# Optimization experiments

Hardware: AMD Instinct MI355X
Metric: run time of the kernel (lower is better)

## Reference

```python
import jax, jax.numpy as jnp
import numpy as np


def setup_inputs() -> dict:
    key = jax.random.key(0)
    k1, k2 = jax.random.split(key)
    x = jax.random.normal(k1, (32, 64, 32, 32), dtype=jnp.float32)
    codebook = jax.random.normal(k2, (2048, 64), dtype=jnp.float32)
    return {"x": x, "codebook": codebook}


def reference(x, codebook):
    B, C, H, W = x.shape
    # (B, C, H, W) -> (B*H*W, C) channels-last flatten
    xf = jnp.transpose(x, (0, 2, 3, 1)).reshape(-1, C)
    d2 = (jnp.sum(xf * xf, axis=-1, keepdims=True)
          + jnp.sum(codebook * codebook, axis=-1)[None, :]
          - 2.0 * jnp.einsum('nc,kc->nk', xf, codebook))
    idx = jnp.argmin(d2, axis=-1)            # (B*H*W,)
    quant = codebook[idx]                    # (B*H*W, C)
    commitment_loss = jnp.mean((jax.lax.stop_gradient(quant) - xf) ** 2)
    codebook_loss = jnp.mean((quant - jax.lax.stop_gradient(xf)) ** 2)
    # Straight-through estimator
    quant_ste = xf + jax.lax.stop_gradient(quant - xf)
    quant_out = jnp.transpose(quant_ste.reshape(B, H, W, C), (0, 3, 1, 2))
    min_encoding_indices = idx.reshape(B, H, W)
    return quant_out, codebook_loss, commitment_loss, min_encoding_indices
```

## Files before the change

### kernel.cpp

```cpp
#include <hip/hip_runtime.h>

#define NROWS    32768
#define KENT     2048
#define OUT_Q_SZ 2097152
#define N_ELEMS  2097152.0f
#define THR      1e-4f
#define KLO      0.001953125f

typedef _Float16 f16x8 __attribute__((ext_vector_type(8)));
typedef float    f32x4 __attribute__((ext_vector_type(4)));

#define WS_LOSS  0
#define WS_CNT   4
#define WS_EN    1024
#define WS_LIST  16384
#define WS_PM1   262144
#define WS_PIX   1310720
#define WS_PM2   2359296

__global__ void vq_norms_kernel(const float* __restrict__ cb, float* __restrict__ ws) {
    int e = blockIdx.x * 256 + threadIdx.x;
    if (e == 0) { ws[0] = 0.0f; ((unsigned*)ws)[1] = 0u; }
    if (e < KENT) {
        const float4* row = (const float4*)(cb + e * 64);
        float s = 0.0f;
#pragma unroll
        for (int i = 0; i < 16; ++i) {
            float4 v = row[i];
            s += v.x * v.x + v.y * v.y + v.z * v.z + v.w * v.w;
        }
        *((float*)((char*)ws + WS_EN) + e) = s;
    }
}

__global__ __launch_bounds__(256, 2) void vq_main_kernel(
    const float* __restrict__ x, const float* __restrict__ cb,
    float* __restrict__ ws)
{
    __shared__ f16x8 a_hi[16 * 2 * 64];
    __shared__ f16x8 a_lo[16 * 2 * 64];
    __shared__ float en_s[256];

    const float*  en  = (const float*)((char*)ws + WS_EN);
    float*        pm1 = (float*)((char*)ws + WS_PM1);
    int*          pix = (int*)  ((char*)ws + WS_PIX);
    float*        pm2 = (float*)((char*)ws + WS_PM2);

    const int tid = threadIdx.x;
    const int rg  = blockIdx.x >> 3;
    const int oct = blockIdx.x & 7;

#pragma unroll
    for (int u = 0; u < 8; ++u) {
        int unit = u * 256 + tid;
        int tile = unit >> 7, step = (unit >> 6) & 1, ln = unit & 63;
        int e  = oct * 256 + tile * 16 + (ln & 15);
        int k0 = step * 32 + ((ln >> 4) << 3);
        float4 v0 = *(const float4*)(cb + e * 64 + k0);
        float4 v1 = *(const float4*)(cb + e * 64 + k0 + 4);
        float vv[8] = {v0.x, v0.y, v0.z, v0.w, v1.x, v1.y, v1.z, v1.w};
        f16x8 h, l;
#pragma unroll
        for (int j = 0; j < 8; ++j) {
            _Float16 hi = (_Float16)vv[j];
            float lo = (vv[j] - (float)hi) * 1024.0f;
            h[j] = hi; l[j] = (_Float16)lo;
        }
        a_hi[unit] = h; a_lo[unit] = l;
    }
    en_s[tid] = en[oct * 256 + tid];
    __syncthreads();

    const int w  = tid >> 6;
    const int ln = tid & 63;
    const int rowbase = rg * 256 + w * 64;

    f16x8 bh[4][2], bl[4][2];
#pragma unroll
    for (int nt = 0; nt < 4; ++nt) {
        int n = rowbase + nt * 16 + (ln & 15);
        const float* xp = x + ((n >> 10) << 16) + (n & 1023);
#pragma unroll
        for (int st = 0; st < 2; ++st) {
            int c0 = st * 32 + ((ln >> 4) << 3);
            f16x8 h, l;
#pragma unroll
            for (int j = 0; j < 8; ++j) {
                float f = xp[(c0 + j) << 10];
                _Float16 hi = (_Float16)f;
                float lo = (f - (float)hi) * 1024.0f;
                h[j] = hi; l[j] = (_Float16)lo;
            }
            bh[nt][st] = h; bl[nt][st] = l;
        }
    }

    float m1[4], m2[4]; int bidx[4];
#pragma unroll
    for (int nt = 0; nt < 4; ++nt) { m1[nt] = 3.4e38f; m2[nt] = 3.4e38f; bidx[nt] = 0; }
    const int ibase = oct * 256 + ((ln >> 4) << 2);

#pragma unroll 1
    for (int tile = 0; tile < 16; ++tile) {
        f16x8 ah0 = a_hi[tile * 128 + ln];
        f16x8 ah1 = a_hi[tile * 128 + 64 + ln];
        f16x8 al0 = a_lo[tile * 128 + ln];
        f16x8 al1 = a_lo[tile * 128 + 64 + ln];
        float4 en4 = *(const float4*)&en_s[tile * 16 + ((ln >> 4) << 2)];
        float env[4] = {en4.x, en4.y, en4.z, en4.w};
        int t4 = ibase + tile * 16;

#pragma unroll
        for (int nt = 0; nt < 4; ++nt) {
            f32x4 z = {0.f, 0.f, 0.f, 0.f};
            f32x4 ah = __builtin_amdgcn_mfma_f32_16x16x32_f16(ah0, bh[nt][0], z, 0, 0, 0);
            ah = __builtin_amdgcn_mfma_f32_16x16x32_f16(ah1, bh[nt][1], ah, 0, 0, 0);
            f32x4 al = __builtin_amdgcn_mfma_f32_16x16x32_f16(ah0, bl[nt][0], z, 0, 0, 0);
            al = __builtin_amdgcn_mfma_f32_16x16x32_f16(ah1, bl[nt][1], al, 0, 0, 0);
            al = __builtin_amdgcn_mfma_f32_16x16x32_f16(al0, bh[nt][0], al, 0, 0, 0);
            al = __builtin_amdgcn_mfma_f32_16x16x32_f16(al1, bh[nt][1], al, 0, 0, 0);
#pragma unroll
            for (int r = 0; r < 4; ++r) {
                float d = fmaf(ah[r], -2.0f, fmaf(al[r], -KLO, env[r]));
                bool lt = d < m1[nt];
                m2[nt] = fminf(m2[nt], fmaxf(d, m1[nt]));
                m1[nt]   = lt ? d : m1[nt];
                bidx[nt] = lt ? (t4 + r) : bidx[nt];
            }
        }
    }

#pragma unroll
    for (int nt = 0; nt < 4; ++nt) {
        float v1 = m1[nt], v2 = m2[nt]; int ix = bidx[nt];
#pragma unroll
        for (int m = 16; m <= 32; m <<= 1) {
            float o1 = __shfl_xor(v1, m, 64);
            int   oi = __shfl_xor(ix, m, 64);
            float o2 = __shfl_xor(v2, m, 64);
            bool lt = (o1 < v1) || (o1 == v1 && oi < ix);
            float loser = lt ? v1 : o1;
            v1 = lt ? o1 : v1; ix = lt ? oi : ix;
            v2 = fminf(loser, fminf(v2, o2));
        }
        if (ln < 16) {
            int row = rowbase + nt * 16 + ln;
            pm1[oct * NROWS + row] = v1;
            pix[oct * NROWS + row] = ix;
            pm2[oct * NROWS + row] = v2;
        }
    }
}

__global__ __launch_bounds__(256) void vq_epilogue_kernel(
    const float* __restrict__ x, const float* __restrict__ cb,
    float* __restrict__ ws, float* __restrict__ out_q, float* __restrict__ out_idx)
{
    __shared__ int idx_s[64];
    __shared__ int flag_s[64];
    __shared__ float wp[4];

    const float* pm1 = (const float*)((char*)ws + WS_PM1);
    const int*   pix = (const int*)  ((char*)ws + WS_PIX);
    const float* pm2 = (const float*)((char*)ws + WS_PM2);
    unsigned*    cnt = (unsigned*)((char*)ws + WS_CNT);
    unsigned*    list = (unsigned*)((char*)ws + WS_LIST);

    const int t = threadIdx.x;
    const int base = blockIdx.x * 64;
    const int b = base >> 10, hw0 = base & 1023;

    if (t < 64) {
        int row = base + t;
        float v1 = 3.4e38f, v2 = 3.4e38f; int ix = 0;
#pragma unroll
        for (int o = 0; o < 8; ++o) {
            float o1 = pm1[o * NROWS + row];
            int   oi = pix[o * NROWS + row];
            float o2 = pm2[o * NROWS + row];
            bool lt = (o1 < v1) || (o1 == v1 && oi < ix);
            float loser = lt ? v1 : o1;
            v1 = lt ? o1 : v1; ix = lt ? oi : ix;
            v2 = fminf(loser, fminf(v2, o2));
        }
        out_idx[row] = (float)ix;
        int fl = (v2 - v1) <= THR;
        idx_s[t] = ix; flag_s[t] = fl;
        if (fl) { unsigned p = atomicAdd(cnt, 1u); list[p] = row; }
    }
    __syncthreads();

    float lsum = 0.0f;
#pragma unroll
    for (int it = 0; it < 16; ++it) {
        int e = it * 256 + t;
        int c = e >> 6, r = e & 63;
        float q  = cb[idx_s[r] * 64 + c];
        float xv = x[(b << 16) + (c << 10) + hw0 + r];
        out_q[(b << 16) + (c << 10) + hw0 + r] = xv + (q - xv);
        float df = q - xv;
        lsum += flag_s[r] ? 0.0f : df * df;
    }
#pragma unroll
    for (int m = 1; m < 64; m <<= 1) lsum += __shfl_xor(lsum, m, 64);
    if ((t & 63) == 0) wp[t >> 6] = lsum;
    __syncthreads();
    if (t == 0) atomicAdd((float*)ws, wp[0] + wp[1] + wp[2] + wp[3]);
}

__global__ __launch_bounds__(256) void vq_fallback_kernel(
    const float* __restrict__ x, const float* __restrict__ cb,
    float* __restrict__ ws, float* __restrict__ out_q, float* __restrict__ out_idx)
{
    __shared__ float x_s[64];
    __shared__ float rd[256];
    __shared__ int   ri[256];

    const float* en  = (const float*)((char*)ws + WS_EN);
    const unsigned F = *(const unsigned*)((char*)ws + WS_CNT);
    const unsigned* list = (const unsigned*)((char*)ws + WS_LIST);
    const int t = threadIdx.x;

    for (unsigned li = blockIdx.x; li < F; li += gridDim.x) {
        int row = list[li];
        int b = row >> 10, hw = row & 1023;
        if (t < 64) x_s[t] = x[(b << 16) + (t << 10) + hw];
        __syncthreads();

        float best = 3.4e38f; int bi = 0;
#pragma unroll 1
        for (int i = 0; i < 8; ++i) {
            int e = i * 256 + t;
            float dot = 0.0f;
#pragma unroll
            for (int c4 = 0; c4 < 16; ++c4) {
                float4 cv = *(const float4*)(cb + e * 64 + c4 * 4);
                float4 xv = *(const float4*)&x_s[c4 * 4];
                dot += cv.x * xv.x + cv.y * xv.y + cv.z * xv.z + cv.w * xv.w;
            }
            float d = en[e] - 2.0f * dot;
            if (d < best) { best = d; bi = e; }
        }
        rd[t] = best; ri[t] = bi;
        __syncthreads();
        for (int s = 128; s > 0; s >>= 1) {
            if (t < s) {
                bool lt = (rd[t + s] < rd[t]) || (rd[t + s] == rd[t] && ri[t + s] < ri[t]);
                if (lt) { rd[t] = rd[t + s]; ri[t] = ri[t + s]; }
            }
            __syncthreads();
        }
        int ix = ri[0];
        if (t == 0) out_idx[row] = (float)ix;
        float lsum = 0.0f;
        if (t < 64) {
            float q = cb[ix * 64 + t];
            float xv = x_s[t];
            out_q[(b << 16) + (t << 10) + hw] = xv + (q - xv);
            float df = q - xv; lsum = df * df;
        }
        if (t < 64) {
#pragma unroll
            for (int m = 1; m < 64; m <<= 1) lsum += __shfl_xor(lsum, m, 64);
            if (t == 0) atomicAdd((float*)ws, lsum);
        }
        __syncthreads();
    }
}

__global__ void vq_finalize_kernel(const float* __restrict__ ws, float* __restrict__ out) {
    float m = ws[0] * (1.0f / N_ELEMS);
    out[OUT_Q_SZ]     = m;
    out[OUT_Q_SZ + 1] = m;
}

extern "C" void kernel_launch(void* const* d_in, const int* in_sizes, int n_in,
                              void* d_out, int out_size, void* d_ws, size_t ws_size,
                              hipStream_t stream) {
    const float* x  = (const float*)d_in[0];
    const float* cb = (const float*)d_in[1];
    float* out = (float*)d_out;
    float* ws  = (float*)d_ws;

    vq_norms_kernel<<<8, 256, 0, stream>>>(cb, ws);
    vq_main_kernel<<<1024, 256, 0, stream>>>(x, cb, ws);
    vq_epilogue_kernel<<<512, 256, 0, stream>>>(x, cb, ws, out, out + OUT_Q_SZ + 2);
    vq_fallback_kernel<<<64, 256, 0, stream>>>(x, cb, ws, out, out + OUT_Q_SZ + 2);
    vq_finalize_kernel<<<1, 1, 0, stream>>>(ws, out);
}
```

Measured before the change: 83.39 us.

## Fuse epilogue into main kernel with 32x32 MFMA and precomputed split codebook

Precomputes the fp16 hi/lo split of the codebook once in a prep kernel, laid out in MFMA fragment order in workspace. The main kernel now gives each 512-thread block 64 rows across the whole codebook, using 32x32x16 MFMAs. It reduces argmin candidates in LDS and writes quantized output, indices and loss directly, so the partial-min buffers and the separate epilogue launch go away. The trade-off is that codebook fragments are read from global/L2 in every block instead of LDS, and there is less parallelism per row.

```diff
diff --git a/kernel.cpp b/kernel.cpp
--- a/kernel.cpp
+++ b/kernel.cpp
@@ -7,205 +7,213 @@
 #define THR      1e-4f
 #define KLO      0.001953125f
 
-typedef _Float16 f16x8 __attribute__((ext_vector_type(8)));
-typedef float    f32x4 __attribute__((ext_vector_type(4)));
+typedef _Float16 f16x8  __attribute__((ext_vector_type(8)));
+typedef float    f32x16 __attribute__((ext_vector_type(16)));
 
 #define WS_LOSS  0
 #define WS_CNT   4
 #define WS_EN    1024
 #define WS_LIST  16384
-#define WS_PM1   262144
-#define WS_PIX   1310720
-#define WS_PM2   2359296
-
-__global__ void vq_norms_kernel(const float* __restrict__ cb, float* __restrict__ ws) {
-    int e = blockIdx.x * 256 + threadIdx.x;
-    if (e == 0) { ws[0] = 0.0f; ((unsigned*)ws)[1] = 0u; }
-    if (e < KENT) {
-        const float4* row = (const float4*)(cb + e * 64);
+#define WS_CBH   262144
+#define WS_CBL   524288
+
+__global__ __launch_bounds__(256) void vq_prep_kernel(
+    const float* __restrict__ cb, float* __restrict__ ws)
+{
+    const int unit = blockIdx.x * 256 + threadIdx.x;
+    if (unit == 0) { ws[0] = 0.0f; ((unsigned*)ws)[1] = 0u; }
+
+    const int gm = unit >> 8, ks = (unit >> 6) & 3, l = unit & 63;
+    const int e  = gm * 32 + (l & 31);
+    const int ch = ks * 16 + ((l >> 5) << 3);
+    float4 v0 = *(const float4*)(cb + e * 64 + ch);
+    float4 v1 = *(const float4*)(cb + e * 64 + ch + 4);
+    float vv[8] = {v0.x, v0.y, v0.z, v0.w, v1.x, v1.y, v1.z, v1.w};
+    f16x8 h, lo;
+#pragma unroll
+    for (int j = 0; j < 8; ++j) {
+        _Float16 hi = (_Float16)vv[j];
+        float r = (vv[j] - (float)hi) * 1024.0f;
+        h[j] = hi; lo[j] = (_Float16)r;
+    }
+    *(f16x8*)((_Float16*)((char*)ws + WS_CBH) + unit * 8) = h;
+    *(f16x8*)((_Float16*)((char*)ws + WS_CBL) + unit * 8) = lo;
+
+    if (unit < KENT) {
+        const float4* row = (const float4*)(cb + unit * 64);
         float s = 0.0f;
 #pragma unroll
         for (int i = 0; i < 16; ++i) {
             float4 v = row[i];
             s += v.x * v.x + v.y * v.y + v.z * v.z + v.w * v.w;
         }
-        *((float*)((char*)ws + WS_EN) + e) = s;
-    }
-}
-
-__global__ __launch_bounds__(256, 2) void vq_main_kernel(
+        *((float*)((char*)ws + WS_EN) + unit) = s;
+    }
+}
+
+__global__ __launch_bounds__(512, 4) void vq_main_kernel(
     const float* __restrict__ x, const float* __restrict__ cb,
-    float* __restrict__ ws)
+    float* __restrict__ ws, float* __restrict__ out_q,
+    float* __restrict__ out_idx)
 {
-    __shared__ f16x8 a_hi[16 * 2 * 64];
-    __shared__ f16x8 a_lo[16 * 2 * 64];
-    __shared__ float en_s[256];
-
-    const float*  en  = (const float*)((char*)ws + WS_EN);
-    float*        pm1 = (float*)((char*)ws + WS_PM1);
-    int*          pix = (int*)  ((char*)ws + WS_PIX);
-    float*        pm2 = (float*)((char*)ws + WS_PM2);
+    __shared__ float lds_x[64 * 68];
+    __shared__ float mb1[64 * 4];
+    __shared__ float mb2[64 * 4];
+    __shared__ int   mbi[64 * 4];
+    __shared__ int   idx_s[64];
+    __shared__ int   flag_s[64];
+    __shared__ float wp[8];
+
+    const float*    en  = (const float*)((char*)ws + WS_EN);
+    const _Float16* cbh = (const _Float16*)((char*)ws + WS_CBH);
+    const _Float16* cbl = (const _Float16*)((char*)ws + WS_CBL);
+    unsigned* cnt  = (unsigned*)((char*)ws + WS_CNT);
+    unsigned* list = (unsigned*)((char*)ws + WS_LIST);
 
     const int tid = threadIdx.x;
-    const int rg  = blockIdx.x >> 3;
-    const int oct = blockIdx.x & 7;
-
-#pragma unroll
-    for (int u = 0; u < 8; ++u) {
-        int unit = u * 256 + tid;
-        int tile = unit >> 7, step = (unit >> 6) & 1, ln = unit & 63;
-        int e  = oct * 256 + tile * 16 + (ln & 15);
-        int k0 = step * 32 + ((ln >> 4) << 3);
-        float4 v0 = *(const float4*)(cb + e * 64 + k0);
-        float4 v1 = *(const float4*)(cb + e * 64 + k0 + 4);
-        float vv[8] = {v0.x, v0.y, v0.z, v0.w, v1.x, v1.y, v1.z, v1.w};
-        f16x8 h, l;
+    const int n0  = blockIdx.x * 64;
+    const int b   = n0 >> 10;
+    const int hw0 = n0 & 1023;
+    const float* xg = x + b * 65536 + hw0;
+
+    {
+        int c = tid >> 3, s = tid & 7;
+        float4 a0 = *(const float4*)(xg + c * 1024 + s * 8);
+        float4 a1 = *(const float4*)(xg + c * 1024 + s * 8 + 4);
+        *(float4*)(&lds_x[c * 68 + s * 8])     = a0;
+        *(float4*)(&lds_x[c * 68 + s * 8 + 4]) = a1;
+    }
+    __syncthreads();
+
+    const int l  = tid & 63;
+    const int wv = tid >> 6;
+    const int rh = wv >> 2;
+    const int eq = wv & 3;
+    const int r0 = rh * 32;
+
+    f16x8 bh[4], bl[4];
+#pragma unroll
+    for (int ks = 0; ks < 4; ++ks) {
+        f16x8 h, lo;
 #pragma unroll
         for (int j = 0; j < 8; ++j) {
-            _Float16 hi = (_Float16)vv[j];
-            float lo = (vv[j] - (float)hi) * 1024.0f;
-            h[j] = hi; l[j] = (_Float16)lo;
-        }
-        a_hi[unit] = h; a_lo[unit] = l;
-    }
-    en_s[tid] = en[oct * 256 + tid];
-    __syncthreads();
-
-    const int w  = tid >> 6;
-    const int ln = tid & 63;
-    const int rowbase = rg * 256 + w * 64;
-
-    f16x8 bh[4][2], bl[4][2];
-#pragma unroll
-    for (int nt = 0; nt < 4; ++nt) {
-        int n = rowbase + nt * 16 + (ln & 15);
-        const float* xp = x + ((n >> 10) << 16) + (n & 1023);
-#pragma unroll
-        for (int st = 0; st < 2; ++st) {
-            int c0 = st * 32 + ((ln >> 4) << 3);
-            f16x8 h, l;
-#pragma unroll
-            for (int j = 0; j < 8; ++j) {
-                float f = xp[(c0 + j) << 10];
-                _Float16 hi = (_Float16)f;
-                float lo = (f - (float)hi) * 1024.0f;
-                h[j] = hi; l[j] = (_Float16)lo;
-            }
-            bh[nt][st] = h; bl[nt][st] = l;
-        }
-    }
-
-    float m1[4], m2[4]; int bidx[4];
-#pragma unroll
-    for (int nt = 0; nt < 4; ++nt) { m1[nt] = 3.4e38f; m2[nt] = 3.4e38f; bidx[nt] = 0; }
-    const int ibase = oct * 256 + ((ln >> 4) << 2);
+            int ch = ks * 16 + ((l >> 5) << 3) + j;
+            float f = lds_x[ch * 68 + r0 + (l & 31)];
+            _Float16 hi = (_Float16)f;
+            float r = (f - (float)hi) * 1024.0f;
+            h[j] = hi; lo[j] = (_Float16)r;
+        }
+        bh[ks] = h; bl[ks] = lo;
+    }
+
+    float m1 = 3.4e38f, m2 = 3.4e38f;
+    int   bix = 0;
+    const int lane_eoff = (l >> 5) << 2;
 
 #pragma unroll 1
-    for (int tile = 0; tile < 16; ++tile) {
-        f16x8 ah0 = a_hi[tile * 128 + ln];
-        f16x8 ah1 = a_hi[tile * 128 + 64 + ln];
-        f16x8 al0 = a_lo[tile * 128 + ln];
-        f16x8 al1 = a_lo[tile * 128 + 64 + ln];
-        float4 en4 = *(const float4*)&en_s[tile * 16 + ((ln >> 4) << 2)];
-        float env[4] = {en4.x, en4.y, en4.z, en4.w};
-        int t4 = ibase + tile * 16;
-
-#pragma unroll
-        for (int nt = 0; nt < 4; ++nt) {
-            f32x4 z = {0.f, 0.f, 0.f, 0.f};
-            f32x4 ah = __builtin_amdgcn_mfma_f32_16x16x32_f16(ah0, bh[nt][0], z, 0, 0, 0);
-            ah = __builtin_amdgcn_mfma_f32_16x16x32_f16(ah1, bh[nt][1], ah, 0, 0, 0);
-            f32x4 al = __builtin_amdgcn_mfma_f32_16x16x32_f16(ah0, bl[nt][0], z, 0, 0, 0);
-            al = __builtin_amdgcn_mfma_f32_16x16x32_f16(ah1, bl[nt][1], al, 0, 0, 0);
-            al = __builtin_amdgcn_mfma_f32_16x16x32_f16(al0, bh[nt][0], al, 0, 0, 0);
-            al = __builtin_amdgcn_mfma_f32_16x16x32_f16(al1, bh[nt][1], al, 0, 0, 0);
-#pragma unroll
-            for (int r = 0; r < 4; ++r) {
-                float d = fmaf(ah[r], -2.0f, fmaf(al[r], -KLO, env[r]));
-                bool lt = d < m1[nt];
-                m2[nt] = fminf(m2[nt], fmaxf(d, m1[nt]));
-                m1[nt]   = lt ? d : m1[nt];
-                bidx[nt] = lt ? (t4 + r) : bidx[nt];
-            }
-        }
-    }
-
-#pragma unroll
-    for (int nt = 0; nt < 4; ++nt) {
-        float v1 = m1[nt], v2 = m2[nt]; int ix = bidx[nt];
-#pragma unroll
-        for (int m = 16; m <= 32; m <<= 1) {
-            float o1 = __shfl_xor(v1, m, 64);
-            int   oi = __shfl_xor(ix, m, 64);
-            float o2 = __shfl_xor(v2, m, 64);
+    for (int m = 0; m < 16; ++m) {
+        const int gm = eq * 16 + m;
+        const _Float16* ap = cbh + ((size_t)(gm * 4) * 64 + l) * 8;
+        const _Float16* lp = cbl + ((size_t)(gm * 4) * 64 + l) * 8;
+        f16x8 ah0 = *(const f16x8*)(ap);
+        f16x8 ah1 = *(const f16x8*)(ap + 512);
+        f16x8 ah2 = *(const f16x8*)(ap + 1024);
+        f16x8 ah3 = *(const f16x8*)(ap + 1536);
+        f16x8 al0 = *(const f16x8*)(lp);
+        f16x8 al1 = *(const f16x8*)(lp + 512);
+        f16x8 al2 = *(const f16x8*)(lp + 1024);
+        f16x8 al3 = *(const f16x8*)(lp + 1536);
+
+        f32x16 z = {0.f,0.f,0.f,0.f,0.f,0.f,0.f,0.f,0.f,0.f,0.f,0.f,0.f,0.f,0.f,0.f};
+        f32x16 acch = __builtin_amdgcn_mfma_f32_32x32x16_f16(ah0, bh[0], z, 0, 0, 0);
+        acch = __builtin_amdgcn_mfma_f32_32x32x16_f16(ah1, bh[1], acch, 0, 0, 0);
+        acch = __builtin_amdgcn_mfma_f32_32x32x16_f16(ah2, bh[2], acch, 0, 0, 0);
+        acch = __builtin_amdgcn_mfma_f32_32x32x16_f16(ah3, bh[3], acch, 0, 0, 0);
+        f32x16 accl = __builtin_amdgcn_mfma_f32_32x32x16_f16(ah0, bl[0], z, 0, 0, 0);
+        accl = __builtin_amdgcn_mfma_f32_32x32x16_f16(ah1, bl[1], accl, 0, 0, 0);
+        accl = __builtin_amdgcn_mfma_f32_32x32x16_f16(ah2, bl[2], accl, 0, 0, 0);
+        accl = __builtin_amdgcn_mfma_f32_32x32x16_f16(ah3, bl[3], accl, 0, 0, 0);
+        accl = __builtin_amdgcn_mfma_f32_32x32x16_f16(al0, bh[0], accl, 0, 0, 0);
+        accl = __builtin_amdgcn_mfma_f32_32x32x16_f16(al1, bh[1], accl, 0, 0, 0);
+        accl = __builtin_amdgcn_mfma_f32_32x32x16_f16(al2, bh[2], accl, 0, 0, 0);
+        accl = __builtin_amdgcn_mfma_f32_32x32x16_f16(al3, bh[3], accl, 0, 0, 0);
+
+        const int ebase = eq * 512 + m * 32 + lane_eoff;
+        const float* ep = en + ebase;
+        float4 e0 = *(const float4*)(ep);
+        float4 e1 = *(const float4*)(ep + 8);
+        float4 e2 = *(const float4*)(ep + 16);
+        float4 e3 = *(const float4*)(ep + 24);
+        float ev[16] = {e0.x,e0.y,e0.z,e0.w, e1.x,e1.y,e1.z,e1.w,
+                        e2.x,e2.y,e2.z,e2.w, e3.x,e3.y,e3.z,e3.w};
+
+#pragma unroll
+        for (int r = 0; r < 16; ++r) {
+            float d = fmaf(acch[r], -2.0f, fmaf(accl[r], -KLO, ev[r]));
+            bool lt = d < m1;
+            m2 = __builtin_amdgcn_fmed3f(d, m1, m2);
+            m1 = fminf(d, m1);
+            bix = lt ? (ebase + ((r >> 2) << 3) + (r & 3)) : bix;
+        }
+    }
+
+    {
+        float o1 = __shfl_xor(m1, 32, 64);
+        float o2 = __shfl_xor(m2, 32, 64);
+        int   oi = __shfl_xor(bix, 32, 64);
+        bool lt = (o1 < m1) || (o1 == m1 && oi < bix);
+        float loser = lt ? m1 : o1;
+        m1 = lt ? o1 : m1; bix = lt ? oi : bix;
+        m2 = fminf(loser, fminf(m2, o2));
+    }
+    if (l < 32) {
+        int row = r0 + l;
+        mb1[row * 4 + eq] = m1;
+        mb2[row * 4 + eq] = m2;
+        mbi[row * 4 + eq] = bix;
+    }
+    __syncthreads();
+
+    if (tid < 64) {
+        float v1 = 3.4e38f, v2 = 3.4e38f; int ix = 0;
+#pragma unroll
+        for (int q = 0; q < 4; ++q) {
+            float o1 = mb1[tid * 4 + q];
+            float o2 = mb2[tid * 4 + q];
+            int   oi = mbi[tid * 4 + q];
             bool lt = (o1 < v1) || (o1 == v1 && oi < ix);
             float loser = lt ? v1 : o1;
             v1 = lt ? o1 : v1; ix = lt ? oi : ix;
             v2 = fminf(loser, fminf(v2, o2));
         }
-        if (ln < 16) {
-            int row = rowbase + nt * 16 + ln;
-            pm1[oct * NROWS + row] = v1;
-            pix[oct * NROWS + row] = ix;
-            pm2[oct * NROWS + row] = v2;
-        }
-    }
-}
-
-__global__ __launch_bounds__(256) void vq_epilogue_kernel(
-    const float* __restrict__ x, const float* __restrict__ cb,
-    float* __restrict__ ws, float* __restrict__ out_q, float* __restrict__ out_idx)
-{
-    __shared__ int idx_s[64];
-    __shared__ int flag_s[64];
-    __shared__ float wp[4];
-
-    const float* pm1 = (const float*)((char*)ws + WS_PM1);
-    const int*   pix = (const int*)  ((char*)ws + WS_PIX);
-    const float* pm2 = (const float*)((char*)ws + WS_PM2);
-    unsigned*    cnt = (unsigned*)((char*)ws + WS_CNT);
-    unsigned*    list = (unsigned*)((char*)ws + WS_LIST);
-
-    const int t = threadIdx.x;
-    const int base = blockIdx.x * 64;
-    const int b = base >> 10, hw0 = base & 1023;
-
-    if (t < 64) {
-        int row = base + t;
-        float v1 = 3.4e38f, v2 = 3.4e38f; int ix = 0;
-#pragma unroll
-        for (int o = 0; o < 8; ++o) {
-            float o1 = pm1[o * NROWS + row];
-            int   oi = pix[o * NROWS + row];
-            float o2 = pm2[o * NROWS + row];
-            bool lt = (o1 < v1) || (o1 == v1 && oi < ix);
-            float loser = lt ? v1 : o1;
-            v1 = lt ? o1 : v1; ix = lt ? oi : ix;
-            v2 = fminf(loser, fminf(v2, o2));
-        }
-        out_idx[row] = (float)ix;
+        out_idx[n0 + tid] = (float)ix;
         int fl = (v2 - v1) <= THR;
-        idx_s[t] = ix; flag_s[t] = fl;
-        if (fl) { unsigned p = atomicAdd(cnt, 1u); list[p] = row; }
+        idx_s[tid] = ix; flag_s[tid] = fl;
+        if (fl) { unsigned p = atomicAdd(cnt, 1u); list[p] = n0 + tid; }
     }
     __syncthreads();
 
     float lsum = 0.0f;
 #pragma unroll
-    for (int it = 0; it < 16; ++it) {
-        int e = it * 256 + t;
+    for (int it = 0; it < 8; ++it) {
+        int e = it * 512 + tid;
         int c = e >> 6, r = e & 63;
         float q  = cb[idx_s[r] * 64 + c];
-        float xv = x[(b << 16) + (c << 10) + hw0 + r];
+        float xv = lds_x[c * 68 + r];
         out_q[(b << 16) + (c << 10) + hw0 + r] = xv + (q - xv);
         float df = q - xv;
         lsum += flag_s[r] ? 0.0f : df * df;
     }
 #pragma unroll
-    for (int m = 1; m < 64; m <<= 1) lsum += __shfl_xor(lsum, m, 64);
-    if ((t & 63) == 0) wp[t >> 6] = lsum;
-    __syncthreads();
-    if (t == 0) atomicAdd((float*)ws, wp[0] + wp[1] + wp[2] + wp[3]);
+    for (int mm = 1; mm < 64; mm <<= 1) lsum += __shfl_xor(lsum, mm, 64);
+    if (l == 0) wp[wv] = lsum;
+    __syncthreads();
+    if (tid == 0) {
+        float s = 0.0f;
+#pragma unroll
+        for (int w = 0; w < 8; ++w) s += wp[w];
+        atomicAdd((float*)ws, s);
+    }
 }
 
 __global__ __launch_bounds__(256) void vq_fallback_kernel(
@@ -216,7 +224,7 @@
     __shared__ float rd[256];
     __shared__ int   ri[256];
 
-    const float* en  = (const float*)((char*)ws + WS_EN);
+    const float* en = (const float*)((char*)ws + WS_EN);
     const unsigned F = *(const unsigned*)((char*)ws + WS_CNT);
     const unsigned* list = (const unsigned*)((char*)ws + WS_LIST);
     const int t = threadIdx.x;
@@ -252,16 +260,14 @@
         }
         int ix = ri[0];
         if (t == 0) out_idx[row] = (float)ix;
-        float lsum = 0.0f;
         if (t < 64) {
             float q = cb[ix * 64 + t];
             float xv = x_s[t];
             out_q[(b << 16) + (t << 10) + hw] = xv + (q - xv);
-            float df = q - xv; lsum = df * df;
-        }
-        if (t < 64) {
-#pragma unroll
-            for (int m = 1; m < 64; m <<= 1) lsum += __shfl_xor(lsum, m, 64);
+            float df = q - xv;
+            float lsum = df * df;
+#pragma unroll
+            for (int mm = 1; mm < 64; mm <<= 1) lsum += __shfl_xor(lsum, mm, 64);
             if (t == 0) atomicAdd((float*)ws, lsum);
         }
         __syncthreads();
@@ -282,9 +288,8 @@
     float* out = (float*)d_out;
     float* ws  = (float*)d_ws;
 
-    vq_norms_kernel<<<8, 256, 0, stream>>>(cb, ws);
-    vq_main_kernel<<<1024, 256, 0, stream>>>(x, cb, ws);
-    vq_epilogue_kernel<<<512, 256, 0, stream>>>(x, cb, ws, out, out + OUT_Q_SZ + 2);
+    vq_prep_kernel<<<64, 256, 0, stream>>>(cb, ws);
+    vq_main_kernel<<<512, 512, 0, stream>>>(x, cb, ws, out, out + OUT_Q_SZ + 2);
     vq_fallback_kernel<<<64, 256, 0, stream>>>(x, cb, ws, out, out + OUT_Q_SZ + 2);
     vq_finalize_kernel<<<1, 1, 0, stream>>>(ws, out);
 }
```

Result: faster. 68.85 us (-17.4%).
